# Kernel optimization log

Hardware: AMD Instinct MI355X
Metric: run time of the kernel (lower is better)

## Reference

```python
import jax, jax.numpy as jnp
import numpy as np

D = 128  # dim_input / kernel_num
S = 1    # support_num
NL, NM, NG = 5, 20, 100

def _norm(x, axis):
    return x / jnp.maximum(jnp.linalg.norm(x, axis=axis, keepdims=True), 1e-12)

def _gather(t, idx):
    # t: (b,n,c), idx: (b,n,k) -> (b,n,k,c)
    return jax.vmap(lambda tb, ib: tb[ib])(t, idx)

def _knn(v, k):
    sq = jnp.sum(v * v, axis=-1)
    d = sq[:, :, None] + sq[:, None, :] - 2.0 * jnp.einsum('bic,bjc->bij', v, v)
    _, idx = jax.lax.top_k(-d, k + 1)
    return idx[:, :, 1:]  # drop self

def _conv_surface(idx, v, dirs):
    nd = _norm(_gather(v, idx) - v[:, :, None, :], -1)                    # (b,n,k,3)
    theta = jax.nn.relu(jnp.einsum('bnkc,cd->bnkd', nd, _norm(dirs, 0)))  # (b,n,k,S*D)
    b, n, k, _ = theta.shape
    theta = theta.reshape(b, n, k, S, D)
    return jnp.sum(jnp.max(theta, axis=2), axis=2)                         # (b,n,D)

def _conv_layer(idx, v, fm, W, bias, dirs):
    nd = _norm(_gather(v, idx) - v[:, :, None, :], -1)
    theta = jax.nn.relu(jnp.einsum('bnkc,cd->bnkd', nd, _norm(dirs, 0)))  # (b,n,k,S*D)
    fo = fm @ W + bias                                                    # (b,n,(S+1)*D)
    fc, fs = fo[..., :D], fo[..., D:]
    fs = _gather(fs, idx)                                                 # (b,n,k,S*D)
    b, n, k, _ = theta.shape
    act = (theta * fs).reshape(b, n, k, S, D)
    return fc + jnp.sum(jnp.max(act, axis=2), axis=2)                     # (b,n,D)

def _bn_relu(x, g, b, eps=1e-5):
    # training-mode BatchNorm1d over (batch, points) per channel, then ReLU
    m = jnp.mean(x, axis=(0, 1))
    v = jnp.var(x, axis=(0, 1))
    return jax.nn.relu((x - m) * jax.lax.rsqrt(v + eps) * g + b)

def setup_inputs() -> dict:
    key = jax.random.key(0)
    ks = jax.random.split(key, 16)
    B, N = 4, 1024
    def u(k, shape, fan):
        s = 1.0 / np.sqrt(fan)
        return jax.random.uniform(k, shape, jnp.float32, -s, s)
    inp = {}
    inp['vertices'] = jax.random.normal(ks[0], (B, N, 3), jnp.float32)
    inp['dirs_l'] = u(ks[1], (3, S * D), S * D)
    inp['dirs_m0'] = u(ks[2], (3, S * D), S * D)
    inp['W_m1'] = u(ks[3], (D, (S + 1) * D), (S + 1) * D)
    inp['b_m1'] = u(ks[4], ((S + 1) * D,), (S + 1) * D)
    inp['dirs_m1'] = u(ks[5], (3, S * D), S * D)
    inp['dirs_g0'] = u(ks[6], (3, S * D), S * D)
    inp['W_g1'] = u(ks[7], (D, (S + 1) * D), (S + 1) * D)
    inp['b_g1'] = u(ks[8], ((S + 1) * D,), (S + 1) * D)
    inp['dirs_g1'] = u(ks[9], (3, S * D), S * D)
    inp['W_g2'] = u(ks[10], (D, (S + 1) * D), (S + 1) * D)
    inp['b_g2'] = u(ks[11], ((S + 1) * D,), (S + 1) * D)
    inp['dirs_g2'] = u(ks[12], (3, S * D), S * D)
    for nm in ['l', 'm0', 'm1', 'g0', 'g1', 'g2']:
        inp['g_' + nm] = jnp.ones((D,), jnp.float32)
        inp['be_' + nm] = jnp.zeros((D,), jnp.float32)
    inp['W_down'] = u(ks[13], (3 * D, 2 * D), 3 * D)
    inp['b_down'] = u(ks[14], (2 * D,), 3 * D)
    return inp

def reference(vertices, dirs_l, dirs_m0, W_m1, b_m1, dirs_m1, dirs_g0, W_g1, b_g1, dirs_g1, W_g2, b_g2, dirs_g2, g_l, be_l, g_m0, be_m0, g_m1, be_m1, g_g0, be_g0, g_g1, be_g1, g_g2, be_g2, W_down, b_down):
    il = _knn(vertices, NL)
    im = _knn(vertices, NM)
    ig = _knn(vertices, NG)
    fm_l = _bn_relu(_conv_surface(il, vertices, dirs_l), g_l, be_l)
    fm_m = _bn_relu(_conv_surface(im, vertices, dirs_m0), g_m0, be_m0)
    fm_m = _bn_relu(_conv_layer(im, vertices, fm_m, W_m1, b_m1, dirs_m1), g_m1, be_m1)
    fm_g = _bn_relu(_conv_surface(ig, vertices, dirs_g0), g_g0, be_g0)
    fm_g = _bn_relu(_conv_layer(ig, vertices, fm_g, W_g1, b_g1, dirs_g1), g_g1, be_g1)
    fm_g = _bn_relu(_conv_layer(ig, vertices, fm_g, W_g2, b_g2, dirs_g2), g_g2, be_g2)
    out = jnp.concatenate((fm_l, fm_m, fm_g), axis=2)                      # (b,n,3D)
    return jax.nn.relu(out @ W_down + b_down)                              # (b,n,2D)
```

## Files before the change

### kernel.cpp

```cpp
#include <hip/hip_runtime.h>
#include <math.h>

typedef unsigned long long u64;

__global__ __launch_bounds__(256) void knnsurf_kernel(
    const float* __restrict__ verts,
    int* __restrict__ idx_out, float* __restrict__ nd_out,
    const float* __restrict__ dl, const float* __restrict__ dm,
    const float* __restrict__ dg,
    float* __restrict__ raw_l, float* __restrict__ raw_m, float* __restrict__ raw_g)
{
    __shared__ float vx[1024], vy[1024], vz[1024], sq[1024];
    __shared__ u64 cand[4][320];
    float* ndsh = (float*)&cand[0][0];
    const int tid = threadIdx.x;
    const int row0 = blockIdx.x * 4;
    const int b = row0 >> 10;
    const float* vb = verts + b * 3072;

    for (int t = tid; t < 3072; t += 256) {
        float v = vb[t];
        int n = t / 3, c = t - n * 3;
        if (c == 0) vx[n] = v; else if (c == 1) vy[n] = v; else vz[n] = v;
    }
    __syncthreads();
    for (int n = tid; n < 1024; n += 256) {
        float x = vx[n], y = vy[n], z = vz[n];
        sq[n] = __fadd_rn(__fadd_rn(__fmul_rn(x, x), __fmul_rn(y, y)),
                          __fmul_rn(z, z));
    }
    __syncthreads();

    const int w = tid >> 6, lane = tid & 63;
    const int row = row0 + w;
    const int n_i = row & 1023;
    const float xi = vx[n_i], yi = vy[n_i], zi = vz[n_i];
    const float sqi = sq[n_i];

    u64 K[16];
    u64 m1 = ~0ULL, m2 = ~0ULL;
#pragma unroll
    for (int t = 0; t < 16; ++t) {
        int j = t * 64 + lane;
        float dot = __fadd_rn(__fadd_rn(__fmul_rn(xi, vx[j]),
                                        __fmul_rn(yi, vy[j])),
                              __fmul_rn(zi, vz[j]));
        float d = __fsub_rn(__fadd_rn(sqi, sq[j]), __fmul_rn(2.0f, dot));
        d = __fadd_rn(d, 0.0f);
        unsigned u = __float_as_uint(d);
        unsigned m = (u & 0x80000000u) ? ~u : (u | 0x80000000u);
        u64 k = ((u64)m << 10) | (unsigned)j;
        K[t] = k;
        bool lt1 = k < m1;
        u64 nm2 = lt1 ? m1 : ((k < m2) ? k : m2);
        m1 = lt1 ? k : m1;
        m2 = nm2;
    }

    u64 tmax = m2, tmin = m1;
#pragma unroll
    for (int off = 1; off < 64; off <<= 1) {
        u64 a = __shfl_xor(tmax, off); if (a > tmax) tmax = a;
        u64 c = __shfl_xor(tmin, off); if (c < tmin) tmin = c;
    }

    u64 T = tmax;
    int chi;
    {
        int c = 0;
#pragma unroll
        for (int t = 0; t < 16; ++t) c += (K[t] < T) ? 1 : 0;
#pragma unroll
        for (int off = 1; off < 64; off <<= 1) c += __shfl_xor(c, off);
        chi = c;
    }
    u64 lo = tmin, hi = T;
    while (chi > 320) {
        u64 mid = (lo + hi) >> 1;
        int c = 0;
#pragma unroll
        for (int t = 0; t < 16; ++t) c += (K[t] < mid) ? 1 : 0;
#pragma unroll
        for (int off = 1; off < 64; off <<= 1) c += __shfl_xor(c, off);
        if (c >= 101) { hi = mid; chi = c; } else lo = mid;
    }
    T = hi;
    const int n = chi;

    int myc_n = 0;
#pragma unroll
    for (int t = 0; t < 16; ++t) myc_n += (K[t] < T) ? 1 : 0;
    int sc = myc_n;
#pragma unroll
    for (int off = 1; off < 64; off <<= 1) {
        int v = __shfl_up(sc, off);
        if (lane >= off) sc += v;
    }
    int pos = sc - myc_n;
#pragma unroll
    for (int t = 0; t < 16; ++t) {
        if (K[t] < T) cand[w][pos++] = K[t];
    }
    __syncthreads();

    u64 myc[5]; int rk[5];
#pragma unroll
    for (int q = 0; q < 5; ++q) {
        int i = lane + q * 64;
        myc[q] = (i < n) ? cand[w][i] : ~0ULL;
        rk[q] = 0;
    }
    for (int jj = 0; jj < n; ++jj) {
        u64 kk = cand[w][jj];
#pragma unroll
        for (int q = 0; q < 5; ++q) rk[q] += (kk < myc[q]) ? 1 : 0;
    }

    const int rowbase = row & ~1023;
    float* nds_w = ndsh + w * 640;
#pragma unroll
    for (int q = 0; q < 5; ++q) {
        int i = lane + q * 64;
        if (i < n) {
            int r = rk[q];
            if (r >= 1 && r <= 100) {
                int slot = r - 1;
                unsigned j = (unsigned)(myc[q] & 1023u);
                idx_out[row * 100 + slot] = rowbase + (int)j;
                float dx = vx[j] - xi, dy = vy[j] - yi, dz = vz[j] - zi;
                float nrm = sqrtf(__fadd_rn(__fadd_rn(__fmul_rn(dx, dx),
                                                      __fmul_rn(dy, dy)),
                                            __fmul_rn(dz, dz)));
                float inv = 1.0f / fmaxf(nrm, 1e-12f);
                float* o = nd_out + (row * 100 + slot) * 3;
                float nx = dx * inv, ny = dy * inv, nz = dz * inv;
                o[0] = nx; o[1] = ny; o[2] = nz;
                nds_w[3 * slot] = nx; nds_w[3 * slot + 1] = ny; nds_w[3 * slot + 2] = nz;
            }
        }
    }
    __syncthreads();

    const int d = tid & 127;
    float lx = dl[d], ly = dl[128 + d], lz = dl[256 + d];
    float li = 1.0f / fmaxf(sqrtf((lx * lx + ly * ly) + lz * lz), 1e-12f);
    lx *= li; ly *= li; lz *= li;
    float mx = dm[d], my = dm[128 + d], mz = dm[256 + d];
    float mi = 1.0f / fmaxf(sqrtf((mx * mx + my * my) + mz * mz), 1e-12f);
    mx *= mi; my *= mi; mz *= mi;
    float gx = dg[d], gy = dg[128 + d], gz = dg[256 + d];
    float gi = 1.0f / fmaxf(sqrtf((gx * gx + gy * gy) + gz * gz), 1e-12f);
    gx *= gi; gy *= gi; gz *= gi;

#pragma unroll
    for (int p = 0; p < 2; ++p) {
        int rr = (tid >> 7) + 2 * p;
        const float* ns = ndsh + rr * 640;
        float ml = -1e30f, mm = -1e30f, mg = -1e30f;
        int k = 0;
        for (; k < 5; ++k) {
            float x = ns[3 * k], y = ns[3 * k + 1], z = ns[3 * k + 2];
            ml = fmaxf(ml, (x * lx + y * ly) + z * lz);
            mm = fmaxf(mm, (x * mx + y * my) + z * mz);
            mg = fmaxf(mg, (x * gx + y * gy) + z * gz);
        }
        for (; k < 20; ++k) {
            float x = ns[3 * k], y = ns[3 * k + 1], z = ns[3 * k + 2];
            mm = fmaxf(mm, (x * mx + y * my) + z * mz);
            mg = fmaxf(mg, (x * gx + y * gy) + z * gz);
        }
        for (; k < 100; ++k) {
            float x = ns[3 * k], y = ns[3 * k + 1], z = ns[3 * k + 2];
            mg = fmaxf(mg, (x * gx + y * gy) + z * gz);
        }
        int orow = row0 + rr;
        raw_l[orow * 128 + d] = fmaxf(ml, 0.0f);
        raw_m[orow * 128 + d] = fmaxf(mm, 0.0f);
        raw_g[orow * 128 + d] = fmaxf(mg, 0.0f);
    }
}

__global__ __launch_bounds__(256) void bnsum_kernel(
    const float* s0, double* p0,
    const float* s1, double* p1,
    const float* s2, double* p2)
{
    const int t = blockIdx.x >> 5;
    const int blk = blockIdx.x & 31;
    const float* src = (t == 0) ? s0 : (t == 1) ? s1 : s2;
    double* p = (t == 0) ? p0 : (t == 1) ? p1 : p2;
    const int tid = threadIdx.x;
    const int c = tid & 127, seg = tid >> 7;
    const float* q = src + ((size_t)blk * 128 + seg * 64) * 128 + c;
    double s = 0.0, ss = 0.0;
    for (int r = 0; r < 64; ++r) { float v = q[r * 128]; s += v; ss += (double)v * v; }
    __shared__ double Ls[2][128], Lq[2][128];
    Ls[seg][c] = s; Lq[seg][c] = ss;
    __syncthreads();
    if (tid < 128) {
        p[blk * 256 + c]       = Ls[0][c] + Ls[1][c];
        p[blk * 256 + 128 + c] = Lq[0][c] + Lq[1][c];
    }
}

__device__ __forceinline__ void compute_st(const double* __restrict__ p,
                                           const float* __restrict__ g,
                                           const float* __restrict__ e,
                                           float* stA, float* stB,
                                           int tid, int nthreads)
{
    for (int c = tid; c < 128; c += nthreads) {
        double S = 0.0, Q = 0.0;
#pragma unroll
        for (int bb = 0; bb < 32; ++bb) { S += p[bb * 256 + c]; Q += p[bb * 256 + 128 + c]; }
        double m = S * (1.0 / 4096.0);
        double var = Q * (1.0 / 4096.0) - m * m;
        double a = (double)g[c] / sqrt(var + 1e-5);
        stA[c] = (float)a;
        stB[c] = (float)((double)e[c] - m * a);
    }
}

__global__ __launch_bounds__(256) void gemm2_kernel(
    const float* __restrict__ Aa, const double* __restrict__ pa,
    const float* __restrict__ ga, const float* __restrict__ ea,
    const float* __restrict__ Wa, const float* __restrict__ ba, float* __restrict__ outa,
    const float* __restrict__ Ab, const double* __restrict__ pb,
    const float* __restrict__ gb, const float* __restrict__ eb,
    const float* __restrict__ Wb, const float* __restrict__ bb, float* __restrict__ outb)
{
    const int job = blockIdx.y;
    const float* A = job ? Ab : Aa;  const double* p = job ? pb : pa;
    const float* g = job ? gb : ga;  const float* e = job ? eb : ea;
    const float* W = job ? Wb : Wa;  const float* bias = job ? bb : ba;
    float* out = job ? outb : outa;

    __shared__ float stA[128], stB[128];
    __shared__ float As[8 * 128];
    const int o = threadIdx.x;
    const int r0 = blockIdx.x * 8;

    compute_st(p, g, e, stA, stB, o, 256);
    __syncthreads();

    for (int t = o; t < 8 * 128; t += 256) {
        int r = t >> 7, c = t & 127;
        As[t] = fmaxf(fmaf(stA[c], A[(r0 + r) * 128 + c], stB[c]), 0.0f);
    }
    __syncthreads();

    float acc[8];
    const float bz = bias[o];
#pragma unroll
    for (int r = 0; r < 8; ++r) acc[r] = bz;

    for (int c = 0; c < 128; c += 4) {
        float w0 = W[(c + 0) * 256 + o];
        float w1 = W[(c + 1) * 256 + o];
        float w2 = W[(c + 2) * 256 + o];
        float w3 = W[(c + 3) * 256 + o];
#pragma unroll
        for (int r = 0; r < 8; ++r) {
            const float4 av = *(const float4*)&As[r * 128 + c];
            acc[r] += av.x * w0 + av.y * w1 + av.z * w2 + av.w * w3;
        }
    }
#pragma unroll
    for (int r = 0; r < 8; ++r)
        out[(r0 + r) * 256 + o] = acc[r];
}

__global__ __launch_bounds__(128) void layer_kernel(
    const float* __restrict__ nd, const int* __restrict__ idxbuf,
    const float* dir0, const float* fo0, float* out0, int K0,
    const float* dir1, const float* fo1, float* out1, int K1)
{
    const int job = blockIdx.y;
    const float* dirs = job ? dir1 : dir0;
    const float* fo = job ? fo1 : fo0;
    float* out = job ? out1 : out0;
    const int K = job ? K1 : K0;

    const int d = threadIdx.x;
    const int row = blockIdx.x;

    float dx = dirs[d], dy = dirs[128 + d], dz = dirs[256 + d];
    float di = 1.0f / fmaxf(sqrtf((dx * dx + dy * dy) + dz * dz), 1e-12f);
    dx *= di; dy *= di; dz *= di;

    const float* ns = nd + (size_t)row * 300;
    const int* ib = idxbuf + (size_t)row * 100;

    float acc = -1e30f;
    for (int k = 0; k < K; ++k) {
        float x = ns[3 * k], y = ns[3 * k + 1], z = ns[3 * k + 2];
        int ix = ib[k];
        float th = fmaxf((x * dx + y * dy) + z * dz, 0.0f);
        float fs = fo[ix * 256 + 128 + d];
        acc = fmaxf(acc, th * fs);
    }
    out[row * 128 + d] = fo[row * 256 + d] + acc;
}

__global__ __launch_bounds__(256) void gemmf_kernel(
    const float* __restrict__ A0, const double* __restrict__ p0,
    const float* __restrict__ g0, const float* __restrict__ e0,
    const float* __restrict__ A1, const double* __restrict__ p1,
    const float* __restrict__ g1, const float* __restrict__ e1,
    const float* __restrict__ A2, const double* __restrict__ p2,
    const float* __restrict__ g2, const float* __restrict__ e2,
    const float* __restrict__ W, const float* __restrict__ bias, float* __restrict__ out)
{
    __shared__ float stA[384], stB[384];
    __shared__ float As[8 * 384];
    const int o = threadIdx.x;
    const int r0 = blockIdx.x * 8;

    compute_st(p0, g0, e0, stA,       stB,       o, 256);
    compute_st(p1, g1, e1, stA + 128, stB + 128, o, 256);
    compute_st(p2, g2, e2, stA + 256, stB + 256, o, 256);
    __syncthreads();

    for (int t = o; t < 8 * 384; t += 256) {
        int r = t / 384, c = t - r * 384;
        int seg = c >> 7, cc = c & 127;
        const float* A = (seg == 0) ? A0 : (seg == 1) ? A1 : A2;
        As[t] = fmaxf(fmaf(stA[c], A[(r0 + r) * 128 + cc], stB[c]), 0.0f);
    }
    __syncthreads();

    float acc[8];
    const float bz = bias[o];
#pragma unroll
    for (int r = 0; r < 8; ++r) acc[r] = bz;

    for (int c = 0; c < 384; c += 4) {
        float w0 = W[(c + 0) * 256 + o];
        float w1 = W[(c + 1) * 256 + o];
        float w2 = W[(c + 2) * 256 + o];
        float w3 = W[(c + 3) * 256 + o];
#pragma unroll
        for (int r = 0; r < 8; ++r) {
            const float4 av = *(const float4*)&As[r * 384 + c];
            acc[r] += av.x * w0 + av.y * w1 + av.z * w2 + av.w * w3;
        }
    }
#pragma unroll
    for (int r = 0; r < 8; ++r)
        out[(r0 + r) * 256 + o] = fmaxf(acc[r], 0.0f);
}

extern "C" void kernel_launch(void* const* d_in, const int* in_sizes, int n_in,
                              void* d_out, int out_size, void* d_ws, size_t ws_size,
                              hipStream_t stream)
{
    (void)in_sizes; (void)n_in; (void)out_size; (void)ws_size;

    const float* verts   = (const float*)d_in[0];
    const float* dirs_l  = (const float*)d_in[1];
    const float* dirs_m0 = (const float*)d_in[2];
    const float* W_m1    = (const float*)d_in[3];
    const float* b_m1    = (const float*)d_in[4];
    const float* dirs_m1 = (const float*)d_in[5];
    const float* dirs_g0 = (const float*)d_in[6];
    const float* W_g1    = (const float*)d_in[7];
    const float* b_g1    = (const float*)d_in[8];
    const float* dirs_g1 = (const float*)d_in[9];
    const float* W_g2    = (const float*)d_in[10];
    const float* b_g2    = (const float*)d_in[11];
    const float* dirs_g2 = (const float*)d_in[12];
    const float* g_l  = (const float*)d_in[13]; const float* be_l  = (const float*)d_in[14];
    const float* g_m0 = (const float*)d_in[15]; const float* be_m0 = (const float*)d_in[16];
    const float* g_m1 = (const float*)d_in[17]; const float* be_m1 = (const float*)d_in[18];
    const float* g_g0 = (const float*)d_in[19]; const float* be_g0 = (const float*)d_in[20];
    const float* g_g1 = (const float*)d_in[21]; const float* be_g1 = (const float*)d_in[22];
    const float* g_g2 = (const float*)d_in[23]; const float* be_g2 = (const float*)d_in[24];
    const float* W_down = (const float*)d_in[25];
    const float* b_down = (const float*)d_in[26];

    char* ws = (char*)d_ws;
    const size_t MB = 1 << 20;
    int*    idx100 = (int*)   (ws + 0);
    double* p_l    = (double*)(ws + 0x1A0000);
    double* p_m0   = p_l  + 8192;
    double* p_m1   = p_m0 + 8192;
    double* p_g0   = p_m1 + 8192;
    double* p_g1   = p_g0 + 8192;
    double* p_g2   = p_g1 + 8192;
    float* nd100  = (float*)(ws +  2 * MB);
    float* raw_l  = (float*)(ws +  8 * MB);
    float* raw_m0 = (float*)(ws + 10 * MB);
    float* raw_g0 = (float*)(ws + 12 * MB);
    float* raw_m1 = (float*)(ws + 14 * MB);
    float* raw_g1 = (float*)(ws + 16 * MB);
    float* raw_g2 = (float*)(ws + 18 * MB);
    float* fo_m   = (float*)(ws + 20 * MB);
    float* fo_g   = (float*)(ws + 24 * MB);
    float* fo_g2  = (float*)(ws + 28 * MB);

    knnsurf_kernel<<<1024, 256, 0, stream>>>(verts, idx100, nd100,
                                             dirs_l, dirs_m0, dirs_g0,
                                             raw_l, raw_m0, raw_g0);
    bnsum_kernel<<<96, 256, 0, stream>>>(raw_l, p_l, raw_m0, p_m0, raw_g0, p_g0);
    gemm2_kernel<<<dim3(512, 2), 256, 0, stream>>>(
        raw_m0, p_m0, g_m0, be_m0, W_m1, b_m1, fo_m,
        raw_g0, p_g0, g_g0, be_g0, W_g1, b_g1, fo_g);
    layer_kernel<<<dim3(4096, 2), 128, 0, stream>>>(nd100, idx100,
                                                    dirs_m1, fo_m, raw_m1, 20,
                                                    dirs_g1, fo_g, raw_g1, 100);
    bnsum_kernel<<<64, 256, 0, stream>>>(raw_m1, p_m1, raw_g1, p_g1, raw_g1, p_g1);
    gemm2_kernel<<<dim3(512, 1), 256, 0, stream>>>(
        raw_g1, p_g1, g_g1, be_g1, W_g2, b_g2, fo_g2,
        raw_g1, p_g1, g_g1, be_g1, W_g2, b_g2, fo_g2);
    layer_kernel<<<dim3(4096, 1), 128, 0, stream>>>(nd100, idx100,
                                                    dirs_g2, fo_g2, raw_g2, 100,
                                                    dirs_g2, fo_g2, raw_g2, 100);
    bnsum_kernel<<<32, 256, 0, stream>>>(raw_g2, p_g2, raw_g2, p_g2, raw_g2, p_g2);
    gemmf_kernel<<<512, 256, 0, stream>>>(raw_l, p_l, g_l, be_l,
                                          raw_m1, p_m1, g_m1, be_m1,
                                          raw_g2, p_g2, g_g2, be_g2,
                                          W_down, b_down, (float*)d_out);
}
```

Measured before the change: 289.0 us.

## Pack vertices and normalized directions as float4 and shrink kNN candidate buffer

Vertices are now stored in shared memory as one float4 per point (x, y, z plus the squared norm), and the normalized neighbor directions are stored as float4 in both shared and global memory. The aim is to replace scattered scalar loads with single vector loads in the knn kernel and in layer_kernel. The candidate cap for the rank-based selection drops from 320 to 192, with a padded sentinel so the ranking loop can read candidates two at a time. This cuts the O(n^2) ranking work and register use, at the price of more bisection steps. The float4 padding raises global traffic for the direction buffer, so workspace offsets move to make room.

Result: faster. 273.8 us (-5.3%).

```diff
diff --git a/kernel.cpp b/kernel.cpp
--- a/kernel.cpp
+++ b/kernel.cpp
@@ -5,47 +5,42 @@
 
 __global__ __launch_bounds__(256) void knnsurf_kernel(
     const float* __restrict__ verts,
-    int* __restrict__ idx_out, float* __restrict__ nd_out,
+    int* __restrict__ idx_out, float4* __restrict__ nd_out,
     const float* __restrict__ dl, const float* __restrict__ dm,
     const float* __restrict__ dg,
     float* __restrict__ raw_l, float* __restrict__ raw_m, float* __restrict__ raw_g)
 {
-    __shared__ float vx[1024], vy[1024], vz[1024], sq[1024];
-    __shared__ u64 cand[4][320];
-    float* ndsh = (float*)&cand[0][0];
+    __shared__ float4 vps[1024];
+    __shared__ __align__(16) u64 cand[4][208];
     const int tid = threadIdx.x;
     const int row0 = blockIdx.x * 4;
     const int b = row0 >> 10;
     const float* vb = verts + b * 3072;
 
-    for (int t = tid; t < 3072; t += 256) {
-        float v = vb[t];
-        int n = t / 3, c = t - n * 3;
-        if (c == 0) vx[n] = v; else if (c == 1) vy[n] = v; else vz[n] = v;
-    }
-    __syncthreads();
     for (int n = tid; n < 1024; n += 256) {
-        float x = vx[n], y = vy[n], z = vz[n];
-        sq[n] = __fadd_rn(__fadd_rn(__fmul_rn(x, x), __fmul_rn(y, y)),
-                          __fmul_rn(z, z));
+        float x = vb[3 * n], y = vb[3 * n + 1], z = vb[3 * n + 2];
+        float s = __fadd_rn(__fadd_rn(__fmul_rn(x, x), __fmul_rn(y, y)),
+                            __fmul_rn(z, z));
+        vps[n] = make_float4(x, y, z, s);
     }
     __syncthreads();
 
     const int w = tid >> 6, lane = tid & 63;
     const int row = row0 + w;
     const int n_i = row & 1023;
-    const float xi = vx[n_i], yi = vy[n_i], zi = vz[n_i];
-    const float sqi = sq[n_i];
+    const float4 pi = vps[n_i];
+    const float xi = pi.x, yi = pi.y, zi = pi.z, sqi = pi.w;
 
     u64 K[16];
     u64 m1 = ~0ULL, m2 = ~0ULL;
 #pragma unroll
     for (int t = 0; t < 16; ++t) {
         int j = t * 64 + lane;
-        float dot = __fadd_rn(__fadd_rn(__fmul_rn(xi, vx[j]),
-                                        __fmul_rn(yi, vy[j])),
-                              __fmul_rn(zi, vz[j]));
-        float d = __fsub_rn(__fadd_rn(sqi, sq[j]), __fmul_rn(2.0f, dot));
+        float4 p = vps[j];
+        float dot = __fadd_rn(__fadd_rn(__fmul_rn(xi, p.x),
+                                        __fmul_rn(yi, p.y)),
+                              __fmul_rn(zi, p.z));
+        float d = __fsub_rn(__fadd_rn(sqi, p.w), __fmul_rn(2.0f, dot));
         d = __fadd_rn(d, 0.0f);
         unsigned u = __float_as_uint(d);
         unsigned m = (u & 0x80000000u) ? ~u : (u | 0x80000000u);
@@ -75,7 +70,7 @@
         chi = c;
     }
     u64 lo = tmin, hi = T;
-    while (chi > 320) {
+    while (chi > 192) {
         u64 mid = (lo + hi) >> 1;
         int c = 0;
 #pragma unroll
@@ -101,25 +96,33 @@
     for (int t = 0; t < 16; ++t) {
         if (K[t] < T) cand[w][pos++] = K[t];
     }
-    __syncthreads();
-
-    u64 myc[5]; int rk[5];
-#pragma unroll
-    for (int q = 0; q < 5; ++q) {
+    if (lane == 0) cand[w][n] = ~0ULL;
+    __syncthreads();
+
+    u64 myc[3]; int rk[3];
+#pragma unroll
+    for (int q = 0; q < 3; ++q) {
         int i = lane + q * 64;
         myc[q] = (i < n) ? cand[w][i] : ~0ULL;
         rk[q] = 0;
     }
-    for (int jj = 0; jj < n; ++jj) {
-        u64 kk = cand[w][jj];
-#pragma unroll
-        for (int q = 0; q < 5; ++q) rk[q] += (kk < myc[q]) ? 1 : 0;
+    {
+        const ulonglong2* c2 = (const ulonglong2*)&cand[w][0];
+        const int half = (n + 1) >> 1;
+        for (int jj = 0; jj < half; ++jj) {
+            ulonglong2 kk = c2[jj];
+#pragma unroll
+            for (int q = 0; q < 3; ++q) {
+                rk[q] += (kk.x < myc[q]) ? 1 : 0;
+                rk[q] += (kk.y < myc[q]) ? 1 : 0;
+            }
+        }
     }
 
     const int rowbase = row & ~1023;
-    float* nds_w = ndsh + w * 640;
-#pragma unroll
-    for (int q = 0; q < 5; ++q) {
+    float4* nd4w = (float4*)&cand[w][0];
+#pragma unroll
+    for (int q = 0; q < 3; ++q) {
         int i = lane + q * 64;
         if (i < n) {
             int r = rk[q];
@@ -127,15 +130,15 @@
                 int slot = r - 1;
                 unsigned j = (unsigned)(myc[q] & 1023u);
                 idx_out[row * 100 + slot] = rowbase + (int)j;
-                float dx = vx[j] - xi, dy = vy[j] - yi, dz = vz[j] - zi;
+                float4 pj = vps[j];
+                float dx = pj.x - xi, dy = pj.y - yi, dz = pj.z - zi;
                 float nrm = sqrtf(__fadd_rn(__fadd_rn(__fmul_rn(dx, dx),
                                                       __fmul_rn(dy, dy)),
                                             __fmul_rn(dz, dz)));
                 float inv = 1.0f / fmaxf(nrm, 1e-12f);
-                float* o = nd_out + (row * 100 + slot) * 3;
-                float nx = dx * inv, ny = dy * inv, nz = dz * inv;
-                o[0] = nx; o[1] = ny; o[2] = nz;
-                nds_w[3 * slot] = nx; nds_w[3 * slot + 1] = ny; nds_w[3 * slot + 2] = nz;
+                float4 nv = make_float4(dx * inv, dy * inv, dz * inv, 0.0f);
+                nd_out[row * 100 + slot] = nv;
+                nd4w[slot] = nv;
             }
         }
     }
@@ -155,23 +158,23 @@
 #pragma unroll
     for (int p = 0; p < 2; ++p) {
         int rr = (tid >> 7) + 2 * p;
-        const float* ns = ndsh + rr * 640;
+        const float4* ns = (const float4*)&cand[rr][0];
         float ml = -1e30f, mm = -1e30f, mg = -1e30f;
         int k = 0;
         for (; k < 5; ++k) {
-            float x = ns[3 * k], y = ns[3 * k + 1], z = ns[3 * k + 2];
-            ml = fmaxf(ml, (x * lx + y * ly) + z * lz);
-            mm = fmaxf(mm, (x * mx + y * my) + z * mz);
-            mg = fmaxf(mg, (x * gx + y * gy) + z * gz);
+            float4 v = ns[k];
+            ml = fmaxf(ml, (v.x * lx + v.y * ly) + v.z * lz);
+            mm = fmaxf(mm, (v.x * mx + v.y * my) + v.z * mz);
+            mg = fmaxf(mg, (v.x * gx + v.y * gy) + v.z * gz);
         }
         for (; k < 20; ++k) {
-            float x = ns[3 * k], y = ns[3 * k + 1], z = ns[3 * k + 2];
-            mm = fmaxf(mm, (x * mx + y * my) + z * mz);
-            mg = fmaxf(mg, (x * gx + y * gy) + z * gz);
+            float4 v = ns[k];
+            mm = fmaxf(mm, (v.x * mx + v.y * my) + v.z * mz);
+            mg = fmaxf(mg, (v.x * gx + v.y * gy) + v.z * gz);
         }
         for (; k < 100; ++k) {
-            float x = ns[3 * k], y = ns[3 * k + 1], z = ns[3 * k + 2];
-            mg = fmaxf(mg, (x * gx + y * gy) + z * gz);
+            float4 v = ns[k];
+            mg = fmaxf(mg, (v.x * gx + v.y * gy) + v.z * gz);
         }
         int orow = row0 + rr;
         raw_l[orow * 128 + d] = fmaxf(ml, 0.0f);
@@ -271,7 +274,7 @@
 }
 
 __global__ __launch_bounds__(128) void layer_kernel(
-    const float* __restrict__ nd, const int* __restrict__ idxbuf,
+    const float4* __restrict__ nd, const int* __restrict__ idxbuf,
     const float* dir0, const float* fo0, float* out0, int K0,
     const float* dir1, const float* fo1, float* out1, int K1)
 {
@@ -288,14 +291,14 @@
     float di = 1.0f / fmaxf(sqrtf((dx * dx + dy * dy) + dz * dz), 1e-12f);
     dx *= di; dy *= di; dz *= di;
 
-    const float* ns = nd + (size_t)row * 300;
+    const float4* ns = nd + (size_t)row * 100;
     const int* ib = idxbuf + (size_t)row * 100;
 
     float acc = -1e30f;
     for (int k = 0; k < K; ++k) {
-        float x = ns[3 * k], y = ns[3 * k + 1], z = ns[3 * k + 2];
+        float4 v = ns[k];
         int ix = ib[k];
-        float th = fmaxf((x * dx + y * dy) + z * dz, 0.0f);
+        float th = fmaxf((v.x * dx + v.y * dy) + v.z * dz, 0.0f);
         float fs = fo[ix * 256 + 128 + d];
         acc = fmaxf(acc, th * fs);
     }
@@ -387,16 +390,16 @@
     double* p_g0   = p_m1 + 8192;
     double* p_g1   = p_g0 + 8192;
     double* p_g2   = p_g1 + 8192;
-    float* nd100  = (float*)(ws +  2 * MB);
-    float* raw_l  = (float*)(ws +  8 * MB);
-    float* raw_m0 = (float*)(ws + 10 * MB);
-    float* raw_g0 = (float*)(ws + 12 * MB);
-    float* raw_m1 = (float*)(ws + 14 * MB);
-    float* raw_g1 = (float*)(ws + 16 * MB);
-    float* raw_g2 = (float*)(ws + 18 * MB);
-    float* fo_m   = (float*)(ws + 20 * MB);
-    float* fo_g   = (float*)(ws + 24 * MB);
-    float* fo_g2  = (float*)(ws + 28 * MB);
+    float4* nd100  = (float4*)(ws + 2 * MB);
+    float* raw_l  = (float*)(ws +  9 * MB);
+    float* raw_m0 = (float*)(ws + 11 * MB);
+    float* raw_g0 = (float*)(ws + 13 * MB);
+    float* raw_m1 = (float*)(ws + 15 * MB);
+    float* raw_g1 = (float*)(ws + 17 * MB);
+    float* raw_g2 = (float*)(ws + 19 * MB);
+    float* fo_m   = (float*)(ws + 21 * MB);
+    float* fo_g   = (float*)(ws + 25 * MB);
+    float* fo_g2  = (float*)(ws + 29 * MB);
 
     knnsurf_kernel<<<1024, 256, 0, stream>>>(verts, idx100, nd100,
                                              dirs_l, dirs_m0, dirs_g0,
```
